# Performance work log

Measured on AMD Instinct MI355X. Metric: run time of the kernel, lower is better.

Reference implementation:

```python
import jax, jax.numpy as jnp
import numpy as np

# shift search range (matches init_kwargs)
MIN_SX, MAX_SX = -4, 4
MIN_SY, MAX_SY = -4, 4
B, C, H, W = 4, 3, 512, 512


def _shift(x, sx, sy):
    """torch.roll on dims (1,2) of a [C,H,W] tensor, zeroing wrapped rows/cols.

    Equivalent to AutomatedShiftFix.shift: positive sx zeros rows [:sx],
    negative sx zeros rows [sx:]; same for sy on the W axis.
    """
    h, w = x.shape[1], x.shape[2]
    shifted = jnp.roll(x, (sx, sy), axis=(1, 2))
    i = jnp.arange(h)[:, None]   # [H,1]
    j = jnp.arange(w)[None, :]   # [1,W]
    mask_h = jnp.where(sx >= 0, i >= sx, i < h + sx)
    mask_w = jnp.where(sy >= 0, j >= sy, j < w + sy)
    mask = (mask_h & mask_w).astype(x.dtype)  # [H,W]
    return shifted * mask[None]


def _all_shifts():
    sx = jnp.arange(MIN_SX, MAX_SX + 1)
    sy = jnp.arange(MIN_SY, MAX_SY + 1)
    # outer loop over shift_x, inner over shift_y -> 'ij' matches torch ordering
    return jnp.stack(jnp.meshgrid(sx, sy, indexing="ij"), axis=-1).reshape(-1, 2)  # [Ns,2]


def setup_inputs() -> dict:
    key = jax.random.key(0)
    k1, k2 = jax.random.split(key)
    x_ref = jax.random.normal(k1, (B, C, H, W), dtype=jnp.float32)
    x = jax.random.normal(k2, (B, C, H, W), dtype=jnp.float32)
    return {"x_ref": x_ref, "x": x}


def reference(x_ref, x):
    shifts = _all_shifts()  # [Ns,2] int32

    def sims_one(xr, xi):  # xr, xi: [C,H,W]
        # similarity for every candidate shift: sum over (C,H,W) of shifted*ref
        return jax.vmap(lambda s: jnp.sum(_shift(xi, s[0], s[1]) * xr))(shifts)  # [Ns]

    sims = jax.vmap(sims_one)(x_ref, x)          # [B, Ns]
    best = jnp.argmax(sims, axis=1)              # [B]
    best_shifts = shifts[best]                   # [B, 2]
    out = jax.vmap(lambda xi, s: _shift(xi, s[0], s[1]))(x, best_shifts)  # [B,C,H,W]
    return out, best_shifts
```

## Files before the change

### kernel.cpp

```cpp
#include <hip/hip_runtime.h>

#define BB 4
#define CC 3
#define HH 512
#define WW 512
#define NS 81
#define IMG (HH * WW)
#define CHW (CC * IMG)
#define RSTRIP 8


__global__ void k_init(double* __restrict__ sims) {
    int i = threadIdx.x;
    if (i < BB * NS) sims[i] = 0.0;
}

__global__ __launch_bounds__(256, 3) void k_sims(const float* __restrict__ xref,
                                                 const float* __restrict__ x,
                                                 double* __restrict__ sims) {
    int bid = blockIdx.x;
    int r0  = (bid & 63) * RSTRIP;
    int bc  = bid >> 6;
    int b   = bc / CC;
    const float* xp = x    + (size_t)bc * IMG;
    const float* rp = xref + (size_t)bc * IMG;
    int tid  = threadIdx.x;
    int lane = tid & 63;
    int wave = tid >> 6;
    int j0   = lane << 3;

    float acc[NS];
#pragma unroll
    for (int s = 0; s < NS; ++s) acc[s] = 0.f;

    for (int p = 0; p < RSTRIP / 4; ++p) {
        int ip = r0 + p * 4 + wave;
        const float* xrow = xp + ip * WW + j0;
        float x8[8];
        *(float4*)(x8)     = *(const float4*)(xrow);
        *(float4*)(x8 + 4) = *(const float4*)(xrow + 4);

#pragma unroll
        for (int sxi = 0; sxi < 9; ++sxi) {
            int ii = ip + sxi - 4;
            if ((unsigned)ii >= HH) continue;
            const float* rrow = rp + ii * WW + j0;
            float w[16];
            if (j0 >= 4) *(float4*)(w) = *(const float4*)(rrow - 4);
            else { w[0] = w[1] = w[2] = w[3] = 0.f; }
            *(float4*)(w + 4) = *(const float4*)(rrow);
            *(float4*)(w + 8) = *(const float4*)(rrow + 4);
            if (j0 + 12 <= WW) *(float4*)(w + 12) = *(const float4*)(rrow + 8);
            else { w[12] = w[13] = w[14] = w[15] = 0.f; }
#pragma unroll
            for (int syi = 0; syi < 9; ++syi)
#pragma unroll
                for (int k = 0; k < 8; ++k)
                    acc[sxi * 9 + syi] += x8[k] * w[k + syi];
        }
    }

    __shared__ float part[4][NS];
#pragma unroll
    for (int s = 0; s < NS; ++s) {
        float v = acc[s];
        for (int off = 32; off; off >>= 1) v += __shfl_down(v, off, 64);
        if (lane == 0) part[wave][s] = v;
    }
    __syncthreads();
    if (tid < NS) {
        double tot = (double)part[0][tid] + (double)part[1][tid]
                   + (double)part[2][tid] + (double)part[3][tid];
        atomicAdd(&sims[b * NS + tid], tot);
    }
}

__global__ void k_argmax(const double* __restrict__ sims,
                         int* __restrict__ best,
                         float* __restrict__ outTail) {
    int b = blockIdx.x;
    int t = threadIdx.x;
    double bv = -1.0e300;
    int bi = NS;
    for (int s = t; s < NS; s += 64) {
        double v = sims[b * NS + s];
        if (v > bv || (v == bv && s < bi)) { bv = v; bi = s; }
    }
    for (int off = 32; off; off >>= 1) {
        double ov = __shfl_down(bv, off, 64);
        int    oi = __shfl_down(bi, off, 64);
        if (ov > bv || (ov == bv && oi < bi)) { bv = ov; bi = oi; }
    }
    if (t == 0) {
        int sx = bi / 9 - 4;
        int sy = bi % 9 - 4;
        best[b * 2]     = sx;
        best[b * 2 + 1] = sy;
        outTail[b * 2]     = (float)sx;
        outTail[b * 2 + 1] = (float)sy;
    }
}

__global__ __launch_bounds__(256) void k_apply(const float* __restrict__ x,
                                               const int* __restrict__ best,
                                               float* __restrict__ out) {
    int idx = blockIdx.x * blockDim.x + threadIdx.x;
    int j0     = (idx % (WW / 4)) * 4;
    int rowIdx = idx / (WW / 4);
    int i  = rowIdx % HH;
    int bc = rowIdx / HH;
    int b  = bc / CC;
    int sx = best[b * 2];
    int sy = best[b * 2 + 1];
    int is = i - sx;
    float4 v = make_float4(0.f, 0.f, 0.f, 0.f);
    if (is >= 0 && is < HH) {
        const float* src = x + (size_t)bc * IMG + is * WW;
        float* vv = (float*)&v;
#pragma unroll
        for (int k = 0; k < 4; ++k) {
            int js = j0 + k - sy;
            if (js >= 0 && js < WW) vv[k] = src[js];
        }
    }
    *(float4*)(out + (size_t)bc * IMG + i * WW + j0) = v;
}

extern "C" void kernel_launch(void* const* d_in, const int* in_sizes, int n_in,
                              void* d_out, int out_size, void* d_ws, size_t ws_size,
                              hipStream_t stream) {
    const float* xref = (const float*)d_in[0];
    const float* x    = (const float*)d_in[1];
    float* out = (float*)d_out;

    double* sims = (double*)d_ws;
    int*    best = (int*)((char*)d_ws + 4096);

    k_init<<<1, 512, 0, stream>>>(sims);

    int simBlocks = BB * CC * (HH / RSTRIP);
    k_sims<<<simBlocks, 256, 0, stream>>>(xref, x, sims);

    k_argmax<<<BB, 64, 0, stream>>>(sims, best, out + (size_t)BB * CHW);

    int applyBlocks = (BB * CHW / 4) / 256;
    k_apply<<<applyBlocks, 256, 0, stream>>>(x, best, out);
}
```

Measured before the change: 120.2 us.

## Split shift-x range across blocks, replace atomics with partials, vectorize apply

The similarity kernel now splits the 9 row shifts into 3 groups handled by separate blocks. That cuts per-thread accumulators from 81 to 27, allowing higher occupancy (launch bounds 6). Double atomics and the init kernel are replaced by per-block float partials, which the argmax kernel reduces in double. The apply kernel uses a float4 load on the aligned interior path. The cost is that x rows are loaded three times, and the argmax kernel does a larger serial reduction over 64 strips per channel.

```diff
diff --git a/kernel.cpp b/kernel.cpp
--- a/kernel.cpp
+++ b/kernel.cpp
@@ -7,21 +7,22 @@
 #define NS 81
 #define IMG (HH * WW)
 #define CHW (CC * IMG)
-#define RSTRIP 8
+#define STRIP 8
+#define NSTRIP (HH / STRIP)
+#define NSXG 3
+#define NBLK (BB * CC * NSTRIP * NSXG)
 
+#define BEST_OFF (NBLK * 27 * sizeof(float))
 
-__global__ void k_init(double* __restrict__ sims) {
-    int i = threadIdx.x;
-    if (i < BB * NS) sims[i] = 0.0;
-}
-
-__global__ __launch_bounds__(256, 3) void k_sims(const float* __restrict__ xref,
+__global__ __launch_bounds__(256, 6) void k_sims(const float* __restrict__ xref,
                                                  const float* __restrict__ x,
-                                                 double* __restrict__ sims) {
-    int bid = blockIdx.x;
-    int r0  = (bid & 63) * RSTRIP;
-    int bc  = bid >> 6;
-    int b   = bc / CC;
+                                                 float* __restrict__ partials) {
+    int bid  = blockIdx.x;
+    int sxg  = bid % NSXG;
+    int tmp  = bid / NSXG;
+    int strip = tmp % NSTRIP;
+    int bc   = tmp / NSTRIP;
+    int r0   = strip * STRIP;
     const float* xp = x    + (size_t)bc * IMG;
     const float* rp = xref + (size_t)bc * IMG;
     int tid  = threadIdx.x;
@@ -29,20 +30,21 @@
     int wave = tid >> 6;
     int j0   = lane << 3;
 
-    float acc[NS];
+    float acc[27];
 #pragma unroll
-    for (int s = 0; s < NS; ++s) acc[s] = 0.f;
+    for (int s = 0; s < 27; ++s) acc[s] = 0.f;
 
-    for (int p = 0; p < RSTRIP / 4; ++p) {
-        int ip = r0 + p * 4 + wave;
+#pragma unroll
+    for (int r = 0; r < 2; ++r) {
+        int ip = r0 + wave * 2 + r;
         const float* xrow = xp + ip * WW + j0;
         float x8[8];
         *(float4*)(x8)     = *(const float4*)(xrow);
         *(float4*)(x8 + 4) = *(const float4*)(xrow + 4);
 
 #pragma unroll
-        for (int sxi = 0; sxi < 9; ++sxi) {
-            int ii = ip + sxi - 4;
+        for (int sxl = 0; sxl < 3; ++sxl) {
+            int ii = ip + sxg * 3 + sxl - 4;
             if ((unsigned)ii >= HH) continue;
             const float* rrow = rp + ii * WW + j0;
             float w[16];
@@ -56,42 +58,47 @@
             for (int syi = 0; syi < 9; ++syi)
 #pragma unroll
                 for (int k = 0; k < 8; ++k)
-                    acc[sxi * 9 + syi] += x8[k] * w[k + syi];
+                    acc[sxl * 9 + syi] += x8[k] * w[k + syi];
         }
     }
 
-    __shared__ float part[4][NS];
+    __shared__ float part[4][27];
 #pragma unroll
-    for (int s = 0; s < NS; ++s) {
+    for (int s = 0; s < 27; ++s) {
         float v = acc[s];
         for (int off = 32; off; off >>= 1) v += __shfl_down(v, off, 64);
         if (lane == 0) part[wave][s] = v;
     }
     __syncthreads();
-    if (tid < NS) {
-        double tot = (double)part[0][tid] + (double)part[1][tid]
-                   + (double)part[2][tid] + (double)part[3][tid];
-        atomicAdd(&sims[b * NS + tid], tot);
-    }
+    if (tid < 27)
+        partials[bid * 27 + tid] = part[0][tid] + part[1][tid]
+                                 + part[2][tid] + part[3][tid];
 }
 
-__global__ void k_argmax(const double* __restrict__ sims,
+__global__ void k_argmax(const float* __restrict__ partials,
                          int* __restrict__ best,
                          float* __restrict__ outTail) {
     int b = blockIdx.x;
     int t = threadIdx.x;
-    double bv = -1.0e300;
-    int bi = NS;
-    for (int s = t; s < NS; s += 64) {
-        double v = sims[b * NS + s];
-        if (v > bv || (v == bv && s < bi)) { bv = v; bi = s; }
+    __shared__ double vals[NS];
+    if (t < NS) {
+        int sxi = t / 9, syi = t % 9;
+        int sxg = sxi / 3;
+        int within = (sxi - sxg * 3) * 9 + syi;
+        double acc = 0.0;
+        for (int c = 0; c < CC; ++c)
+            for (int st = 0; st < NSTRIP; ++st) {
+                int pb = ((b * CC + c) * NSTRIP + st) * NSXG + sxg;
+                acc += (double)partials[pb * 27 + within];
+            }
+        vals[t] = acc;
     }
-    for (int off = 32; off; off >>= 1) {
-        double ov = __shfl_down(bv, off, 64);
-        int    oi = __shfl_down(bi, off, 64);
-        if (ov > bv || (ov == bv && oi < bi)) { bv = ov; bi = oi; }
-    }
+    __syncthreads();
     if (t == 0) {
+        double bv = vals[0];
+        int bi = 0;
+        for (int s = 1; s < NS; ++s)
+            if (vals[s] > bv) { bv = vals[s]; bi = s; }
         int sx = bi / 9 - 4;
         int sy = bi % 9 - 4;
         best[b * 2]     = sx;
@@ -104,26 +111,31 @@
 __global__ __launch_bounds__(256) void k_apply(const float* __restrict__ x,
                                                const int* __restrict__ best,
                                                float* __restrict__ out) {
-    int idx = blockIdx.x * blockDim.x + threadIdx.x;
-    int j0     = (idx % (WW / 4)) * 4;
-    int rowIdx = idx / (WW / 4);
-    int i  = rowIdx % HH;
-    int bc = rowIdx / HH;
-    int b  = bc / CC;
-    int sx = best[b * 2];
-    int sy = best[b * 2 + 1];
-    int is = i - sx;
+    int blk = blockIdx.x;
+    int bc  = blk >> 8;
+    int tid = threadIdx.x;
+    int row = ((blk & 255) << 1) + (tid >> 7);
+    int j0  = (tid & 127) << 2;
+    int b   = bc / CC;
+    int sx  = best[b * 2];
+    int sy  = best[b * 2 + 1];
+    int is  = row - sx;
     float4 v = make_float4(0.f, 0.f, 0.f, 0.f);
-    if (is >= 0 && is < HH) {
+    if ((unsigned)is < HH) {
         const float* src = x + (size_t)bc * IMG + is * WW;
-        float* vv = (float*)&v;
+        int js0 = j0 - sy;
+        if (js0 >= 0 && js0 + 3 < WW) {
+            v = *(const float4*)(src + js0);
+        } else {
+            float* vv = (float*)&v;
 #pragma unroll
-        for (int k = 0; k < 4; ++k) {
-            int js = j0 + k - sy;
-            if (js >= 0 && js < WW) vv[k] = src[js];
+            for (int k = 0; k < 4; ++k) {
+                int js = js0 + k;
+                if ((unsigned)js < WW) vv[k] = src[js];
+            }
         }
     }
-    *(float4*)(out + (size_t)bc * IMG + i * WW + j0) = v;
+    *(float4*)(out + (size_t)bc * IMG + row * WW + j0) = v;
 }
 
 extern "C" void kernel_launch(void* const* d_in, const int* in_sizes, int n_in,
@@ -133,16 +145,13 @@
     const float* x    = (const float*)d_in[1];
     float* out = (float*)d_out;
 
-    double* sims = (double*)d_ws;
-    int*    best = (int*)((char*)d_ws + 4096);
+    float* partials = (float*)d_ws;
+    int*   best     = (int*)((char*)d_ws + BEST_OFF);
 
-    k_init<<<1, 512, 0, stream>>>(sims);
+    k_sims<<<NBLK, 256, 0, stream>>>(xref, x, partials);
 
-    int simBlocks = BB * CC * (HH / RSTRIP);
-    k_sims<<<simBlocks, 256, 0, stream>>>(xref, x, sims);
+    k_argmax<<<BB, 128, 0, stream>>>(partials, best, out + (size_t)BB * CHW);
 
-    k_argmax<<<BB, 64, 0, stream>>>(sims, best, out + (size_t)BB * CHW);
-
-    int applyBlocks = (BB * CHW / 4) / 256;
+    int applyBlocks = (BB * CC * HH) / 2;
     k_apply<<<applyBlocks, 256, 0, stream>>>(x, best, out);
 }
```

New measurement: 113.9 us. -5.2%, faster.
